# Kernel tuning notes

Hardware: AMD Instinct MI355X
Metric: run time of the kernel (lower is better)

## Reference

```python
import jax, jax.numpy as jnp
import numpy as np
from math import factorial, pi

LMAX = 6      # max angular momentum
NMAX = 5      # max radial index
RC = 3.0      # PolyCut cutoff radius
UNIT = RC / 3.0

_one = np.ones((LMAX + 1, LMAX + 1), np.float32)
YR = jnp.asarray(2.0 * np.tril(_one) - np.eye(LMAX + 1, dtype=np.float32))
YI = jnp.asarray(2.0 * np.triu(_one, k=1))


def _nlm(l, m):
    return float(np.sqrt((2 * l + 1) / (4 * pi) * factorial(l - m) / factorial(l + m)))


def ylm_mat(v):
    """Solid harmonics r^l Y_lm for one point v=(x,y,z).
    Layout (as in AutoForce sph_repr): Re Y_l^m at [l, l-m]; Im Y_l^m at [l-m, l] for m>0,
    so YR (2*tril-eye) weights real parts (m=0 on the diagonal, weight 1) and
    YI (2*triu(1)) weights imaginary parts, reproducing the m-sum of the power spectrum."""
    x, y, z = v[0], v[1], v[2]
    r2 = x * x + y * y + z * z
    # (x + i y)^m by recursion
    A = [jnp.ones((), v.dtype)]
    B = [jnp.zeros((), v.dtype)]
    for m in range(1, LMAX + 1):
        A.append(x * A[m - 1] - y * B[m - 1])
        B.append(x * B[m - 1] + y * A[m - 1])
    # Pi_l^m(z, r^2): homogeneous associated-Legendre part of degree l-m
    Pi = {(0, 0): jnp.ones((), v.dtype)}
    for m in range(1, LMAX + 1):
        Pi[(m, m)] = (2 * m - 1) * Pi[(m - 1, m - 1)]  # (2m-1)!!
    for m in range(0, LMAX):
        Pi[(m + 1, m)] = (2 * m + 1) * z * Pi[(m, m)]
        for l in range(m + 2, LMAX + 1):
            Pi[(l, m)] = ((2 * l - 1) * z * Pi[(l - 1, m)]
                          - (l + m - 1) * r2 * Pi[(l - 2, m)]) / (l - m)
    Y = jnp.zeros((LMAX + 1, LMAX + 1), v.dtype)
    for l in range(LMAX + 1):
        for m in range(l + 1):
            cnl = _nlm(l, m)
            Y = Y.at[l, l - m].set(cnl * Pi[(l, m)] * A[m])
            if m > 0:
                Y = Y.at[l - m, l].set(cnl * Pi[(l, m)] * B[m])
    return Y


def radial(dist):
    # PolyCut: (1 - d/rc)^2 inside rc, and its derivative
    step = (dist < RC).astype(dist.dtype)
    t = 1.0 - dist / RC
    return step * t * t, -2.0 * step * t / RC


def setup_inputs() -> dict:
    key = jax.random.key(0)
    coo = jax.random.normal(key, (150000, 3), dtype=jnp.float32)
    return {"coo": coo}


def reference(coo):
    xyz = coo / UNIT                                   # (N, 3)
    d = jnp.sqrt(jnp.sum(xyz * xyz, axis=-1))          # (N,)
    n = 2.0 * jnp.arange(NMAX + 1, dtype=coo.dtype)    # even powers 0,2,...,2*nmax
    r, dr = radial(UNIT * d)
    dr = UNIT * dr
    f = r[None] * d[None] ** n[:, None]                # (nmax+1, N)
    Y = jnp.transpose(jax.vmap(ylm_mat)(xyz), (1, 2, 0))                   # (L+1, L+1, N)
    dY = jnp.transpose(jax.vmap(jax.jacfwd(ylm_mat))(xyz), (1, 2, 0, 3))   # (L+1, L+1, N, 3)
    c = jnp.einsum('nj,lmj->nlm', f, Y)                # (nmax+1, L+1, L+1)
    # p[i,k,l] = sum_m YR[l,m]*c[i,l,m]*c[k,l,m] + sum_m YI[m,l]*c[i,m,l]*c[k,m,l]
    p = (jnp.einsum('ilm,klm,lm->ikl', c, c, YR)
         + jnp.einsum('iml,kml,ml->ikl', c, c, YI))    # (nmax+1, nmax+1, L+1)
    # hand-derived gradient chain, as in the torch module
    df = dr[None] * d[None] ** n[:, None] + r[None] * n[:, None] * d[None] ** (n[:, None] - 1.0)
    dfv = df[..., None] * xyz / d[:, None]             # (nmax+1, N, 3)
    dc = (dfv[:, None, None] * Y[None, ..., None]
          + f[:, None, None, :, None] * dY[None])      # (nmax+1, L+1, L+1, N, 3)
    # dp without materializing dnnp: contract dc with (c*YR) / (c*YI) directly
    cYr = c * YR
    cYi = c * YI
    dp = (jnp.einsum('klm,ilmjx->ikljx', cYr, dc)
          + jnp.einsum('ilm,klmjx->ikljx', cYr, dc)
          + jnp.einsum('kml,imljx->ikljx', cYi, dc)
          + jnp.einsum('iml,kmljx->ikljx', cYi, dc))   # (nmax+1, nmax+1, L+1, N, 3)
    return p, dp / UNIT
```

## Files before the change

kernel.cpp:

```cpp
#include <hip/hip_runtime.h>


#define LMAXV 6
#define NSZ 6
#define RCV 3.0f

typedef float float4v __attribute__((ext_vector_type(4)));

__device__ __forceinline__ void barrier_lds() {
    asm volatile("s_waitcnt lgkmcnt(0)" ::: "memory");
    __builtin_amdgcn_sched_barrier(0);
    __builtin_amdgcn_s_barrier();
}

constexpr double csqrt_(double x) {
    double y = x > 1.0 ? x : 1.0;
    for (int i = 0; i < 100; ++i) y = 0.5 * (y + x / y);
    return y;
}
constexpr double factd_(int n) { double r = 1.0; for (int i = 2; i <= n; ++i) r *= i; return r; }
constexpr double PI_D = 3.14159265358979323846;
struct CnlT { float v[7][7]; };
constexpr CnlT make_cnl_() {
    CnlT t{};
    for (int l = 0; l <= 6; ++l)
        for (int m = 0; m <= 6; ++m)
            t.v[l][m] = (m <= l)
                ? (float)csqrt_((2.0 * l + 1.0) / (4.0 * PI_D) * factd_(l - m) / factd_(l + m))
                : 0.0f;
    return t;
}
__device__ constexpr CnlT CNL = make_cnl_();
__device__ constexpr float DFACT[7] = {1.f, 1.f, 3.f, 15.f, 105.f, 945.f, 10395.f};
struct IctT { float v[7][7]; };
constexpr IctT make_ict_() {
    IctT t{};
    for (int l = 0; l <= 6; ++l)
        for (int m = 0; m <= 6; ++m)
            t.v[l][m] = (l > m) ? (float)(1.0 / (double)(l - m)) : 1.0f;
    return t;
}
__device__ constexpr IctT ICT = make_ict_();

__global__ void k_zero(float* __restrict__ cws) {
    int t = blockIdx.x * blockDim.x + threadIdx.x;
    if (t < NSZ * 49) cws[t] = 0.0f;
}

__global__ __launch_bounds__(256) void k_creduce(const float* __restrict__ coo,
                                                 float* __restrict__ cws, int N) {
    const int i_rad = blockIdx.y;
    float acc[7][7];
#pragma unroll
    for (int a = 0; a < 7; ++a)
#pragma unroll
        for (int b = 0; b < 7; ++b) acc[a][b] = 0.0f;

    const int stride = gridDim.x * blockDim.x;
    for (int j = blockIdx.x * blockDim.x + threadIdx.x; j < N; j += stride) {
        float x = coo[3 * j + 0], y = coo[3 * j + 1], z = coo[3 * j + 2];
        float r2 = x * x + y * y + z * z;
        float dn = sqrtf(r2);
        float tt = 1.0f - dn * (1.0f / RCV);
        float r  = (dn < RCV) ? tt * tt : 0.0f;
        float fi = r;
        for (int q = 0; q < i_rad; ++q) fi *= r2;

        float Av[7], Bv[7];
        Av[0] = 1.0f; Bv[0] = 0.0f;
#pragma unroll
        for (int m = 1; m <= 6; ++m) {
            Av[m] = x * Av[m - 1] - y * Bv[m - 1];
            Bv[m] = x * Bv[m - 1] + y * Av[m - 1];
        }

        float P1[7], P2[7];
#pragma unroll
        for (int l = 0; l <= 6; ++l) {
            float PC[7];
#pragma unroll
            for (int mm = 0; mm <= l; ++mm) {
                float pv;
                if (mm == l)            pv = DFACT[l];
                else if (mm == l - 1)   pv = (float)(2 * l - 1) * z * P1[mm];
                else {
                    float a = (float)(2 * l - 1), b = (float)(l + mm - 1);
                    pv = (a * z * P1[mm] - b * r2 * P2[mm]) * (1.0f / (float)(l - mm));
                }
                PC[mm] = pv;
                float base = fi * CNL.v[l][mm] * pv;
                acc[l][l - mm] += base * Av[mm];
                if (mm >= 1) acc[l - mm][l] += base * Bv[mm];
            }
#pragma unroll
            for (int mm = 0; mm <= l; ++mm) { P2[mm] = P1[mm]; P1[mm] = PC[mm]; }
        }
    }

    __shared__ float sblk[49];
    if (threadIdx.x < 49) sblk[threadIdx.x] = 0.0f;
    __syncthreads();
    const int lane = threadIdx.x & 63;
#pragma unroll
    for (int a = 0; a < 7; ++a)
#pragma unroll
        for (int b = 0; b < 7; ++b) {
            float v = acc[a][b];
            v += __shfl_down(v, 32);
            v += __shfl_down(v, 16);
            v += __shfl_down(v, 8);
            v += __shfl_down(v, 4);
            v += __shfl_down(v, 2);
            v += __shfl_down(v, 1);
            if (lane == 0) atomicAdd(&sblk[a * 7 + b], v);
        }
    __syncthreads();
    if (threadIdx.x < 49) atomicAdd(&cws[i_rad * 49 + threadIdx.x], sblk[threadIdx.x]);
}

__global__ void k_p(const float* __restrict__ cws, float* __restrict__ out) {
    int t = threadIdx.x;
    if (t >= 252) return;
    int i = t / 42, k = (t / 7) % 6, l = t % 7;
    const float* ci = cws + i * 49;
    const float* ck = cws + k * 49;
    float s = 0.0f;
    for (int mm = 0; mm <= l; ++mm) {
        float w = (mm == 0) ? 1.0f : 2.0f;
        s += w * ci[l * 7 + (l - mm)] * ck[l * 7 + (l - mm)];
        if (mm >= 1) s += 2.0f * ci[(l - mm) * 7 + l] * ck[(l - mm) * 7 + l];
    }
    out[t] = s;
}

__global__ __launch_bounds__(256) void k_dp(const float* __restrict__ coo,
                                            const float* __restrict__ cws,
                                            float* __restrict__ out, int N,
                                            int nblk) {
    __shared__ float sRe[7][7][6];
    __shared__ float sIm[7][7][6];
    __shared__ float stage[12][768];

    for (int s = threadIdx.x; s < 294; s += blockDim.x) {
        int k = s % 6; int lm = s / 6; int l = lm / 7; int mm = lm % 7;
        float re = 0.0f, im = 0.0f;
        if (mm <= l)            re = ((mm == 0) ? 1.0f : 2.0f) * cws[k * 49 + l * 7 + (l - mm)];
        if (mm >= 1 && mm <= l) im = 2.0f * cws[k * 49 + (l - mm) * 7 + l];
        sRe[l][mm][k] = re;
        sIm[l][mm][k] = im;
    }
    __syncthreads();

    int chunk;
    {
        const int b = blockIdx.x;
        const int q = nblk >> 3, rr = nblk & 7;
        const int xcd = b & 7, idx = b >> 3;
        chunk = (xcd < rr ? xcd * (q + 1) : rr * (q + 1) + (xcd - rr) * q) + idx;
    }
    const int j0 = chunk * 256;
    const int jj = min(j0 + (int)threadIdx.x, N - 1);

    const float x = coo[3 * jj + 0], y = coo[3 * jj + 1], z = coo[3 * jj + 2];
    const float r2 = x * x + y * y + z * z;
    const float dn = sqrtf(r2);
    const float invd = 1.0f / dn;
    const float inv2r2 = 0.5f / r2;
    const float tt = 1.0f - dn * (1.0f / RCV);
    const bool  ins = dn < RCV;
    const float r  = ins ? tt * tt : 0.0f;
    const float dr = ins ? (-2.0f / RCV) * tt : 0.0f;
    const float ux = x * invd, uy = y * invd, uz = z * invd;

    float f[NSZ], dfi[NSZ];
    {
        float p2 = 1.0f;
#pragma unroll
        for (int i = 0; i < NSZ; ++i) {
            f[i] = r * p2;
            dfi[i] = p2 * (dr + (float)(2 * i) * r * invd);
            p2 *= r2;
        }
    }

    float Av[7], Bv[7];
    Av[0] = 1.0f; Bv[0] = 0.0f;
#pragma unroll
    for (int m = 1; m <= 6; ++m) {
        Av[m] = x * Av[m - 1] - y * Bv[m - 1];
        Bv[m] = x * Bv[m - 1] + y * Av[m - 1];
    }

    float P1v[7], P1z[7], P2v[7], P2z[7];
#pragma unroll
    for (int mm = 0; mm < 7; ++mm) {
        P1v[mm] = 0.f; P1z[mm] = 0.f; P2v[mm] = 0.f; P2z[mm] = 0.f;
    }

    const uint32_t sliceB = (uint32_t)N * 12u;
    const uint32_t j0b    = (uint32_t)j0 * 12u;
    const uint32_t remB   = (uint32_t)(min(256, N - j0)) * 12u;
    char* const outB = (char*)out;
    const int tid3 = (int)threadIdx.x * 3;

#pragma unroll 1
    for (int l = 0; l <= LMAXV; ++l) {
        float S[NSZ], Tx[NSZ], Ty[NSZ], Tz[NSZ];
#pragma unroll
        for (int k = 0; k < NSZ; ++k) { S[k] = 0.0f; Tx[k] = 0.0f; Ty[k] = 0.0f; Tz[k] = 0.0f; }

        const float lf  = (float)l;
        const float a2l = 2.0f * lf - 1.0f;
        const float dfl = DFACT[l];

#pragma unroll
        for (int mm = 0; mm <= 6; ++mm) {
            if (mm <= l) {
                const float b  = lf + (float)(mm - 1);
                const float ic = ICT.v[l][mm];
                float pv = (a2l * z * P1v[mm] - b * r2 * P2v[mm]) * ic;
                float pz = (a2l * (P1v[mm] + z * P1z[mm]) - b * r2 * P2z[mm]) * ic;
                if (mm == l) pv = dfl;
                const float pr = ((lf - (float)mm) * pv - z * pz) * inv2r2;
                P2v[mm] = P1v[mm]; P2z[mm] = P1z[mm];
                P1v[mm] = pv; P1z[mm] = pz;

                const float c0  = CNL.v[l][mm];
                const float cp  = c0 * pv;
                const float prx = c0 * 2.0f * pr;
                const float gz  = c0 * pz + prx * z;
                const float pmv = cp * (float)mm;
                const int  mp  = (mm > 0) ? mm - 1 : 0;

                const float ReV = cp * Av[mm];
                const float ReX = prx * x * Av[mm] + pmv * Av[mp];
                const float ReG = prx * y * Av[mm] - pmv * Bv[mp];
                const float ReZ = gz * Av[mm];
#pragma unroll
                for (int k = 0; k < NSZ; ++k) {
                    const float cc = sRe[l][mm][k];
                    S[k]  += cc * ReV;
                    Tx[k] += cc * ReX;
                    Ty[k] += cc * ReG;
                    Tz[k] += cc * ReZ;
                }
                if (mm >= 1) {
                    const float ImV = cp * Bv[mm];
                    const float ImX = prx * x * Bv[mm] + pmv * Bv[mp];
                    const float ImG = prx * y * Bv[mm] + pmv * Av[mp];
                    const float ImZ = gz * Bv[mm];
#pragma unroll
                    for (int k = 0; k < NSZ; ++k) {
                        const float cc = sIm[l][mm][k];
                        S[k]  += cc * ImV;
                        Tx[k] += cc * ImX;
                        Ty[k] += cc * ImG;
                        Tz[k] += cc * ImZ;
                    }
                }
            }
        }

        const uint32_t lbase = 1008u + (uint32_t)l * sliceB + j0b;
        const uint32_t ikstride = 7u * sliceB;
#pragma unroll
        for (int g = 0; g < 3; ++g) {
#pragma unroll
            for (int sl = 0; sl < 12; ++sl) {
                const int s = g * 12 + sl;
                const int i = s / 6, k = s % 6;
                const int a = (i < k) ? i : k;
                const int c = (i < k) ? k : i;
                const float gg = dfi[a] * S[c] + dfi[c] * S[a];
                const float ox = ux * gg + f[a] * Tx[c] + f[c] * Tx[a];
                const float oy = uy * gg + f[a] * Ty[c] + f[c] * Ty[a];
                const float oz = uz * gg + f[a] * Tz[c] + f[c] * Tz[a];
                stage[sl][tid3 + 0] = ox;
                stage[sl][tid3 + 1] = oy;
                stage[sl][tid3 + 2] = oz;
            }
            barrier_lds();
#pragma unroll
            for (int it = 0; it < 9; ++it) {
                const int slot = it * 256 + (int)threadIdx.x;
                const int sl   = slot / 192;
                const int pos  = slot - sl * 192;
                const uint32_t boff = (uint32_t)pos << 4;
                if (boff < remB) {
                    const int s = g * 12 + sl;
                    float4v v = *(const float4v*)&stage[sl][pos << 2];
                    *(float4v*)(outB + lbase + (uint32_t)s * ikstride + boff) = v;
                }
            }
            barrier_lds();
        }
    }
}

extern "C" void kernel_launch(void* const* d_in, const int* in_sizes, int n_in,
                              void* d_out, int out_size, void* d_ws, size_t ws_size,
                              hipStream_t stream) {
    const float* coo = (const float*)d_in[0];
    float* out = (float*)d_out;
    float* cws = (float*)d_ws;
    const int N = in_sizes[0] / 3;

    hipLaunchKernelGGL(k_zero, dim3(1), dim3(320), 0, stream, cws);
    hipLaunchKernelGGL(k_creduce, dim3(128, 6), dim3(256), 0, stream, coo, cws, N);
    hipLaunchKernelGGL(k_p, dim3(1), dim3(256), 0, stream, cws, out);
    const int nb = (N + 255) / 256;
    hipLaunchKernelGGL(k_dp, dim3(nb), dim3(256), 0, stream, coo, cws, out, N, nb);
}
```

Measured before the change: 141.9 us.

## Drop LDS staging in dp kernel; keep all l accumulators in registers and store directly

```diff
diff --git a/kernel.cpp b/kernel.cpp
--- a/kernel.cpp
+++ b/kernel.cpp
@@ -5,12 +5,12 @@
 #define NSZ 6
 #define RCV 3.0f
 
-typedef float float4v __attribute__((ext_vector_type(4)));
-
-__device__ __forceinline__ void barrier_lds() {
-    asm volatile("s_waitcnt lgkmcnt(0)" ::: "memory");
-    __builtin_amdgcn_sched_barrier(0);
-    __builtin_amdgcn_s_barrier();
+typedef float float3v __attribute__((ext_vector_type(3)));
+
+__device__ __forceinline__ int xcd_chunk(int b, int nblk) {
+    const int q = nblk >> 3, rr = nblk & 7;
+    const int xcd = b & 7, idx = b >> 3;
+    return (xcd < rr ? xcd * (q + 1) : rr * (q + 1) + (xcd - rr) * q) + idx;
 }
 
 constexpr double csqrt_(double x) {
@@ -32,15 +32,6 @@
 }
 __device__ constexpr CnlT CNL = make_cnl_();
 __device__ constexpr float DFACT[7] = {1.f, 1.f, 3.f, 15.f, 105.f, 945.f, 10395.f};
-struct IctT { float v[7][7]; };
-constexpr IctT make_ict_() {
-    IctT t{};
-    for (int l = 0; l <= 6; ++l)
-        for (int m = 0; m <= 6; ++m)
-            t.v[l][m] = (l > m) ? (float)(1.0 / (double)(l - m)) : 1.0f;
-    return t;
-}
-__device__ constexpr IctT ICT = make_ict_();
 
 __global__ void k_zero(float* __restrict__ cws) {
     int t = blockIdx.x * blockDim.x + threadIdx.x;
@@ -139,8 +130,6 @@
                                             int nblk) {
     __shared__ float sRe[7][7][6];
     __shared__ float sIm[7][7][6];
-    __shared__ float stage[12][768];
-
     for (int s = threadIdx.x; s < 294; s += blockDim.x) {
         int k = s % 6; int lm = s / 6; int l = lm / 7; int mm = lm % 7;
         float re = 0.0f, im = 0.0f;
@@ -151,27 +140,96 @@
     }
     __syncthreads();
 
-    int chunk;
-    {
-        const int b = blockIdx.x;
-        const int q = nblk >> 3, rr = nblk & 7;
-        const int xcd = b & 7, idx = b >> 3;
-        chunk = (xcd < rr ? xcd * (q + 1) : rr * (q + 1) + (xcd - rr) * q) + idx;
-    }
+    const int chunk = xcd_chunk(blockIdx.x, nblk);
     const int j0 = chunk * 256;
-    const int jj = min(j0 + (int)threadIdx.x, N - 1);
+    const int jglob = j0 + (int)threadIdx.x;
+    const bool active = jglob < N;
+    const int jj = active ? jglob : (N - 1);
 
     const float x = coo[3 * jj + 0], y = coo[3 * jj + 1], z = coo[3 * jj + 2];
     const float r2 = x * x + y * y + z * z;
     const float dn = sqrtf(r2);
     const float invd = 1.0f / dn;
     const float inv2r2 = 0.5f / r2;
+
+    float Av[7], Bv[7];
+    Av[0] = 1.0f; Bv[0] = 0.0f;
+#pragma unroll
+    for (int m = 1; m <= 6; ++m) {
+        Av[m] = x * Av[m - 1] - y * Bv[m - 1];
+        Bv[m] = x * Bv[m - 1] + y * Av[m - 1];
+    }
+
+    float S[7][NSZ], TX[7][NSZ], TY[7][NSZ], TZ[7][NSZ];
+#pragma unroll
+    for (int l = 0; l < 7; ++l)
+#pragma unroll
+        for (int k = 0; k < NSZ; ++k) { S[l][k] = 0.f; TX[l][k] = 0.f; TY[l][k] = 0.f; TZ[l][k] = 0.f; }
+
+    {
+        float P1v[7], P1z[7], P2v[7], P2z[7];
+#pragma unroll
+        for (int mm = 0; mm < 7; ++mm) { P1v[mm] = 0.f; P1z[mm] = 0.f; P2v[mm] = 0.f; P2z[mm] = 0.f; }
+
+#pragma unroll
+        for (int l = 0; l <= LMAXV; ++l) {
+            const float lf  = (float)l;
+            const float a2l = 2.0f * lf - 1.0f;
+#pragma unroll
+            for (int mm = 0; mm <= 6; ++mm) {
+                if (mm <= l) {
+                    const float b  = lf + (float)(mm - 1);
+                    const float ic = (l > mm) ? (1.0f / (float)(l - mm)) : 1.0f;
+                    float pv = (a2l * z * P1v[mm] - b * r2 * P2v[mm]) * ic;
+                    float pz = (a2l * (P1v[mm] + z * P1z[mm]) - b * r2 * P2z[mm]) * ic;
+                    if (mm == l) pv = DFACT[l];
+                    const float pr = ((lf - (float)mm) * pv - z * pz) * inv2r2;
+                    P2v[mm] = P1v[mm]; P2z[mm] = P1z[mm];
+                    P1v[mm] = pv; P1z[mm] = pz;
+
+                    const float c0  = CNL.v[l][mm];
+                    const float cp  = c0 * pv;
+                    const float prx = c0 * 2.0f * pr;
+                    const float gz  = c0 * pz + prx * z;
+                    const float pmv = cp * (float)mm;
+                    const int  mp  = (mm > 0) ? mm - 1 : 0;
+
+                    const float ReV = cp * Av[mm];
+                    const float ReX = prx * x * Av[mm] + pmv * Av[mp];
+                    const float ReG = prx * y * Av[mm] - pmv * Bv[mp];
+                    const float ReZ = gz * Av[mm];
+#pragma unroll
+                    for (int k = 0; k < NSZ; ++k) {
+                        const float cc = sRe[l][mm][k];
+                        S[l][k]  += cc * ReV;
+                        TX[l][k] += cc * ReX;
+                        TY[l][k] += cc * ReG;
+                        TZ[l][k] += cc * ReZ;
+                    }
+                    if (mm >= 1) {
+                        const float ImV = cp * Bv[mm];
+                        const float ImX = prx * x * Bv[mm] + pmv * Bv[mp];
+                        const float ImG = prx * y * Bv[mm] + pmv * Av[mp];
+                        const float ImZ = gz * Bv[mm];
+#pragma unroll
+                        for (int k = 0; k < NSZ; ++k) {
+                            const float cc = sIm[l][mm][k];
+                            S[l][k]  += cc * ImV;
+                            TX[l][k] += cc * ImX;
+                            TY[l][k] += cc * ImG;
+                            TZ[l][k] += cc * ImZ;
+                        }
+                    }
+                }
+            }
+        }
+    }
+
     const float tt = 1.0f - dn * (1.0f / RCV);
     const bool  ins = dn < RCV;
     const float r  = ins ? tt * tt : 0.0f;
     const float dr = ins ? (-2.0f / RCV) * tt : 0.0f;
     const float ux = x * invd, uy = y * invd, uz = z * invd;
-
     float f[NSZ], dfi[NSZ];
     {
         float p2 = 1.0f;
@@ -183,116 +241,25 @@
         }
     }
 
-    float Av[7], Bv[7];
-    Av[0] = 1.0f; Bv[0] = 0.0f;
-#pragma unroll
-    for (int m = 1; m <= 6; ++m) {
-        Av[m] = x * Av[m - 1] - y * Bv[m - 1];
-        Bv[m] = x * Bv[m - 1] + y * Av[m - 1];
-    }
-
-    float P1v[7], P1z[7], P2v[7], P2z[7];
-#pragma unroll
-    for (int mm = 0; mm < 7; ++mm) {
-        P1v[mm] = 0.f; P1z[mm] = 0.f; P2v[mm] = 0.f; P2z[mm] = 0.f;
-    }
+    if (!active) return;
 
     const uint32_t sliceB = (uint32_t)N * 12u;
-    const uint32_t j0b    = (uint32_t)j0 * 12u;
-    const uint32_t remB   = (uint32_t)(min(256, N - j0)) * 12u;
     char* const outB = (char*)out;
-    const int tid3 = (int)threadIdx.x * 3;
-
-#pragma unroll 1
-    for (int l = 0; l <= LMAXV; ++l) {
-        float S[NSZ], Tx[NSZ], Ty[NSZ], Tz[NSZ];
-#pragma unroll
-        for (int k = 0; k < NSZ; ++k) { S[k] = 0.0f; Tx[k] = 0.0f; Ty[k] = 0.0f; Tz[k] = 0.0f; }
-
-        const float lf  = (float)l;
-        const float a2l = 2.0f * lf - 1.0f;
-        const float dfl = DFACT[l];
-
-#pragma unroll
-        for (int mm = 0; mm <= 6; ++mm) {
-            if (mm <= l) {
-                const float b  = lf + (float)(mm - 1);
-                const float ic = ICT.v[l][mm];
-                float pv = (a2l * z * P1v[mm] - b * r2 * P2v[mm]) * ic;
-                float pz = (a2l * (P1v[mm] + z * P1z[mm]) - b * r2 * P2z[mm]) * ic;
-                if (mm == l) pv = dfl;
-                const float pr = ((lf - (float)mm) * pv - z * pz) * inv2r2;
-                P2v[mm] = P1v[mm]; P2z[mm] = P1z[mm];
-                P1v[mm] = pv; P1z[mm] = pz;
-
-                const float c0  = CNL.v[l][mm];
-                const float cp  = c0 * pv;
-                const float prx = c0 * 2.0f * pr;
-                const float gz  = c0 * pz + prx * z;
-                const float pmv = cp * (float)mm;
-                const int  mp  = (mm > 0) ? mm - 1 : 0;
-
-                const float ReV = cp * Av[mm];
-                const float ReX = prx * x * Av[mm] + pmv * Av[mp];
-                const float ReG = prx * y * Av[mm] - pmv * Bv[mp];
-                const float ReZ = gz * Av[mm];
-#pragma unroll
-                for (int k = 0; k < NSZ; ++k) {
-                    const float cc = sRe[l][mm][k];
-                    S[k]  += cc * ReV;
-                    Tx[k] += cc * ReX;
-                    Ty[k] += cc * ReG;
-                    Tz[k] += cc * ReZ;
-                }
-                if (mm >= 1) {
-                    const float ImV = cp * Bv[mm];
-                    const float ImX = prx * x * Bv[mm] + pmv * Bv[mp];
-                    const float ImG = prx * y * Bv[mm] + pmv * Av[mp];
-                    const float ImZ = gz * Bv[mm];
-#pragma unroll
-                    for (int k = 0; k < NSZ; ++k) {
-                        const float cc = sIm[l][mm][k];
-                        S[k]  += cc * ImV;
-                        Tx[k] += cc * ImX;
-                        Ty[k] += cc * ImG;
-                        Tz[k] += cc * ImZ;
-                    }
-                }
-            }
-        }
-
-        const uint32_t lbase = 1008u + (uint32_t)l * sliceB + j0b;
-        const uint32_t ikstride = 7u * sliceB;
-#pragma unroll
-        for (int g = 0; g < 3; ++g) {
-#pragma unroll
-            for (int sl = 0; sl < 12; ++sl) {
-                const int s = g * 12 + sl;
-                const int i = s / 6, k = s % 6;
-                const int a = (i < k) ? i : k;
-                const int c = (i < k) ? k : i;
-                const float gg = dfi[a] * S[c] + dfi[c] * S[a];
-                const float ox = ux * gg + f[a] * Tx[c] + f[c] * Tx[a];
-                const float oy = uy * gg + f[a] * Ty[c] + f[c] * Ty[a];
-                const float oz = uz * gg + f[a] * Tz[c] + f[c] * Tz[a];
-                stage[sl][tid3 + 0] = ox;
-                stage[sl][tid3 + 1] = oy;
-                stage[sl][tid3 + 2] = oz;
-            }
-            barrier_lds();
-#pragma unroll
-            for (int it = 0; it < 9; ++it) {
-                const int slot = it * 256 + (int)threadIdx.x;
-                const int sl   = slot / 192;
-                const int pos  = slot - sl * 192;
-                const uint32_t boff = (uint32_t)pos << 4;
-                if (boff < remB) {
-                    const int s = g * 12 + sl;
-                    float4v v = *(const float4v*)&stage[sl][pos << 2];
-                    *(float4v*)(outB + lbase + (uint32_t)s * ikstride + boff) = v;
-                }
-            }
-            barrier_lds();
+    uint32_t off = 1008u + (uint32_t)jglob * 12u;
+#pragma unroll
+    for (int ik = 0; ik < 36; ++ik) {
+        const int i = ik / 6, k = ik % 6;
+        const int a = (i < k) ? i : k;
+        const int c = (i < k) ? k : i;
+#pragma unroll
+        for (int l = 0; l < 7; ++l) {
+            const float gg = dfi[a] * S[l][c] + dfi[c] * S[l][a];
+            float3v v;
+            v.x = ux * gg + f[a] * TX[l][c] + f[c] * TX[l][a];
+            v.y = uy * gg + f[a] * TY[l][c] + f[c] * TY[l][a];
+            v.z = uz * gg + f[a] * TZ[l][c] + f[c] * TZ[l][a];
+            *(float3v*)(outB + off) = v;
+            off += sliceB;
         }
     }
 }
@@ -304,10 +271,10 @@
     float* out = (float*)d_out;
     float* cws = (float*)d_ws;
     const int N = in_sizes[0] / 3;
+    const int nb = (N + 255) / 256;
 
     hipLaunchKernelGGL(k_zero, dim3(1), dim3(320), 0, stream, cws);
     hipLaunchKernelGGL(k_creduce, dim3(128, 6), dim3(256), 0, stream, coo, cws, N);
     hipLaunchKernelGGL(k_p, dim3(1), dim3(256), 0, stream, cws, out);
-    const int nb = (N + 255) / 256;
     hipLaunchKernelGGL(k_dp, dim3(nb), dim3(256), 0, stream, coo, cws, out, N, nb);
 }
```

Result: slower. 232.0 us (+63.5%).
